# Kernel tuning notes

Measured on AMD Instinct MI355X. Metric: run time of the kernel, lower is better.

## Reference

```python
import math
import jax, jax.numpy as jnp
import numpy as np

ALPHA = 1000.0
N_LAMBDA = 1.0


def setup_inputs() -> dict:
    key = jax.random.key(0)
    k1, k2 = jax.random.split(key)
    xyz1 = jax.random.normal(k1, (4, 8192, 3), dtype=jnp.float32)  # prediction
    xyz2 = jax.random.normal(k2, (4, 8192, 3), dtype=jnp.float32)  # ground truth
    return {"xyz1": xyz1, "xyz2": xyz2}


def _nn(a, b):
    """For each point in a [B,Na,3], squared dist + index of nearest point in b [B,Nb,3]."""
    a2 = jnp.sum(a * a, axis=-1)[:, :, None]          # [B,Na,1]
    b2 = jnp.sum(b * b, axis=-1)[:, None, :]          # [B,1,Nb]
    d = a2 + b2 - 2.0 * jnp.einsum('bnd,bmd->bnm', a, b)  # [B,Na,Nb]
    return jnp.min(d, axis=-1), jnp.argmin(d, axis=-1)


def reference(xyz1, xyz2):
    B, n_x, _ = xyz1.shape
    n_gt = xyz2.shape[1]
    frac_21 = n_gt / n_x

    # torch code calls ChamferFunction.apply(xyz2, xyz1):
    # dist1/idx1 are for gt points (idx1 indexes into xyz1, range n_x),
    # dist2/idx2 are for pred points (idx2 indexes into xyz2, range n_gt).
    dist1, idx1 = _nn(xyz2, xyz1)   # [B, n_gt]
    dist2, idx2 = _nn(xyz1, xyz2)   # [B, n_x]

    exp_dist1 = jnp.exp(-dist1 * ALPHA)
    exp_dist2 = jnp.exp(-dist2 * ALPHA)

    batch = jnp.arange(B)[:, None]

    # how many gt points picked each pred point
    count1 = jnp.zeros((B, n_x), jnp.int32).at[batch, idx1].add(1)
    weight1 = jnp.take_along_axis(count1, idx1, axis=1).astype(jnp.float32) ** N_LAMBDA
    weight1 = 1.0 / jnp.maximum(frac_21 / weight1 + 1e-6, 1.0)
    loss1 = jnp.mean(1.0 - exp_dist1 * weight1, axis=1)

    # how many pred points picked each gt point
    count2 = jnp.zeros((B, n_gt), jnp.int32).at[batch, idx2].add(1)
    weight2 = jnp.take_along_axis(count2, idx2, axis=1).astype(jnp.float32) ** N_LAMBDA
    weight2 = 1.0 / (math.ceil(frac_21) * weight2 + 1e-6)
    loss2 = jnp.mean(1.0 - exp_dist2 * weight2, axis=1)

    return jnp.mean((loss1 + loss2) / 2.0)
```

## Files before the change

kernel.cpp:

```cpp
#include <hip/hip_runtime.h>
#include <cstdint>
#include <cstddef>

#define BATCH 4
#define NPTS 8192
#define CHUNK 128
#define BLOCK 256
#define QPT 8
#define QPB (BLOCK * QPT)
#define NKEYS (2 * BATCH * NPTS)

typedef float v2f __attribute__((ext_vector_type(2)));

__device__ __forceinline__ float halfnorm(float px, float py, float pz) {
    return 0.5f * fmaf(pz, pz, fmaf(py, py, px * px));
}
__device__ __forceinline__ float score(float qx, float qy, float qz,
                                       float px, float py, float pz, float ph) {
    float t = fmaf(-qx, px, ph);
    t = fmaf(-qy, py, t);
    return fmaf(-qz, pz, t);
}
__device__ __forceinline__ unsigned int mono_f32(float f) {
    unsigned int u = __float_as_uint(f);
    return u ^ (unsigned int)(((int)u >> 31) | 0x80000000);
}

__global__ void __launch_bounds__(BLOCK, 4) nn_kernel(
        const float* __restrict__ xyz1,
        const float* __restrict__ xyz2,
        unsigned long long* __restrict__ keys,
        unsigned int* __restrict__ counts,
        float* __restrict__ esum,
        float* __restrict__ out) {
    __shared__ float lx[CHUNK];
    __shared__ float ly[CHUNK];
    __shared__ float lz[CHUNK];
    __shared__ float lh[CHUNK];

    const int tid = threadIdx.x;
    const int qt  = blockIdx.x;
    const int ct  = blockIdx.y;
    const int zb  = blockIdx.z;
    const int b   = zb & 3;
    const int dir = zb >> 2;
    const float* q_ptr = (dir == 0) ? xyz2 : xyz1;
    const float* d_ptr = (dir == 0) ? xyz1 : xyz2;
    const int chunk0 = ct * CHUNK;

    {
        const int fid = (((zb * 64 + ct) * 4 + qt) * BLOCK) + tid;
        if (fid < NKEYS) {
            counts[fid] = 0u;
            esum[fid]   = 0.0f;
        }
        if (fid == 0) out[0] = 1.0f;
    }

    if (tid < 32) {
        const float4* g4 = (const float4*)(d_ptr + (size_t)(b * NPTS + chunk0) * 3);
        float4 t0 = g4[3 * tid + 0];
        float4 t1 = g4[3 * tid + 1];
        float4 t2 = g4[3 * tid + 2];
        float px[4] = {t0.x, t0.w, t1.z, t2.y};
        float py[4] = {t0.y, t1.x, t1.w, t2.z};
        float pz[4] = {t0.z, t1.y, t2.x, t2.w};
#pragma unroll
        for (int i = 0; i < 4; ++i) {
            lx[4 * tid + i] = px[i];
            ly[4 * tid + i] = py[i];
            lz[4 * tid + i] = pz[i];
            lh[4 * tid + i] = halfnorm(px[i], py[i], pz[i]);
        }
    }

    const int qbase = qt * QPB + tid;
    float qx[QPT], qy[QPT], qz[QPT];
#pragma unroll
    for (int u = 0; u < QPT; ++u) {
        const float* qp = q_ptr + (size_t)(b * NPTS + qbase + u * BLOCK) * 3;
        qx[u] = qp[0]; qy[u] = qp[1]; qz[u] = qp[2];
    }

    __syncthreads();

    float bd[QPT];
    int   bj[QPT];
#pragma unroll
    for (int u = 0; u < QPT; ++u) { bd[u] = 3.4e38f; bj[u] = 0; }

#pragma unroll 2
    for (int j = 0; j < CHUNK; j += 8) {
        float4 xa = *(const float4*)(lx + j);
        float4 xb = *(const float4*)(lx + j + 4);
        float4 ya = *(const float4*)(ly + j);
        float4 yb = *(const float4*)(ly + j + 4);
        float4 za = *(const float4*)(lz + j);
        float4 zb4 = *(const float4*)(lz + j + 4);
        float4 ha = *(const float4*)(lh + j);
        float4 hb = *(const float4*)(lh + j + 4);
        v2f x01 = {xa.x, xa.y}, x23 = {xa.z, xa.w}, x45 = {xb.x, xb.y}, x67 = {xb.z, xb.w};
        v2f y01 = {ya.x, ya.y}, y23 = {ya.z, ya.w}, y45 = {yb.x, yb.y}, y67 = {yb.z, yb.w};
        v2f z01 = {za.x, za.y}, z23 = {za.z, za.w}, z45 = {zb4.x, zb4.y}, z67 = {zb4.z, zb4.w};
        v2f h01 = {ha.x, ha.y}, h23 = {ha.z, ha.w}, h45 = {hb.x, hb.y}, h67 = {hb.z, hb.w};

#pragma unroll
        for (int u = 0; u < QPT; ++u) {
            const v2f nqx = {-qx[u], -qx[u]};
            const v2f nqy = {-qy[u], -qy[u]};
            const v2f nqz = {-qz[u], -qz[u]};
            v2f s01 = __builtin_elementwise_fma(nqx, x01, h01);
            v2f s23 = __builtin_elementwise_fma(nqx, x23, h23);
            v2f s45 = __builtin_elementwise_fma(nqx, x45, h45);
            v2f s67 = __builtin_elementwise_fma(nqx, x67, h67);
            s01 = __builtin_elementwise_fma(nqy, y01, s01);
            s23 = __builtin_elementwise_fma(nqy, y23, s23);
            s45 = __builtin_elementwise_fma(nqy, y45, s45);
            s67 = __builtin_elementwise_fma(nqy, y67, s67);
            s01 = __builtin_elementwise_fma(nqz, z01, s01);
            s23 = __builtin_elementwise_fma(nqz, z23, s23);
            s45 = __builtin_elementwise_fma(nqz, z45, s45);
            s67 = __builtin_elementwise_fma(nqz, z67, s67);

            float m0 = fminf(fminf(s01.x, s01.y), s23.x);
            float m1 = fminf(fminf(s23.y, s45.x), s45.y);
            float m2 = fminf(fminf(s67.x, s67.y), m0);
            float m  = fminf(m1, m2);
            if (m < bd[u]) { bd[u] = m; bj[u] = j; }
        }
    }

    const size_t base = ((size_t)zb) * NPTS;
#pragma unroll
    for (int u = 0; u < QPT; ++u) {
        unsigned long long key =
            ((unsigned long long)mono_f32(bd[u]) << 32) |
            (unsigned int)(chunk0 + bj[u]);
        atomicMin(&keys[base + qbase + u * BLOCK], key);
    }
}

__global__ void __launch_bounds__(BLOCK) mid_kernel(
        const float* __restrict__ xyz1,
        const float* __restrict__ xyz2,
        const unsigned long long* __restrict__ keys,
        unsigned int* __restrict__ counts,
        float* __restrict__ esum) {
    const int gtid = blockIdx.x * BLOCK + threadIdx.x;
    const int group = gtid >> 13;
    const int q   = gtid & (NPTS - 1);
    const int b   = group & 3;
    const int dir = group >> 2;
    const float* q_ptr = (dir == 0) ? xyz2 : xyz1;
    const float* d_ptr = (dir == 0) ? xyz1 : xyz2;

    const unsigned long long key = keys[gtid];
    const unsigned int smin_m = (unsigned int)(key >> 32);
    const int gbase = ((int)(unsigned int)key) & (NPTS - 8);

    const float* qp = q_ptr + (size_t)(b * NPTS + q) * 3;
    const float qx = qp[0], qy = qp[1], qz = qp[2];

    const float4* g4 = (const float4*)(d_ptr + (size_t)(b * NPTS + gbase) * 3);
    float4 t0 = g4[0], t1 = g4[1], t2 = g4[2], t3 = g4[3], t4 = g4[4], t5 = g4[5];
    float px[8] = {t0.x, t0.w, t1.z, t2.y, t3.x, t3.w, t4.z, t5.y};
    float py[8] = {t0.y, t1.x, t1.w, t2.z, t3.y, t4.x, t4.w, t5.z};
    float pz[8] = {t0.z, t1.y, t2.x, t2.w, t3.z, t4.y, t5.x, t5.w};

    int r = 0;
    float sx = px[0], sy = py[0], sz = pz[0];
#pragma unroll
    for (int k = 7; k >= 0; --k) {
        float ph = halfnorm(px[k], py[k], pz[k]);
        float s  = score(qx, qy, qz, px[k], py[k], pz[k], ph);
        if (mono_f32(s) == smin_m) { r = k; sx = px[k]; sy = py[k]; sz = pz[k]; }
    }
    const int idx = gbase + r;

    const float dx = qx - sx, dy = qy - sy, dz = qz - sz;
    const float d = dx * dx + dy * dy + dz * dz;
    const float e = expf(-1000.0f * d);

    atomicAdd(&counts[(size_t)group * NPTS + idx], 1u);
    atomicAdd(&esum[(size_t)group * NPTS + idx], e);
}

__global__ void __launch_bounds__(BLOCK) final_kernel(
        const unsigned int* __restrict__ counts,
        const float* __restrict__ esum,
        float* __restrict__ out) {
    __shared__ float red[4];
    const int gtid = blockIdx.x * BLOCK + threadIdx.x;
    const int dir = gtid >> 15;

    const float c = (float)counts[gtid];
    const float e = esum[gtid];
    float w;
    if (dir == 0) w = 1.0f / fmaxf(1.0f / c + 1e-6f, 1.0f);
    else          w = 1.0f / (c + 1e-6f);
    float term = -w * e;

#pragma unroll
    for (int off = 32; off > 0; off >>= 1)
        term += __shfl_down(term, off);
    const int lane = threadIdx.x & 63;
    const int wid  = threadIdx.x >> 6;
    if (lane == 0) red[wid] = term;
    __syncthreads();
    if (threadIdx.x == 0) {
        float t = red[0] + red[1] + red[2] + red[3];
        atomicAdd(out, t * (1.0f / 65536.0f));
    }
}

extern "C" void kernel_launch(void* const* d_in, const int* in_sizes, int n_in,
                              void* d_out, int out_size, void* d_ws, size_t ws_size,
                              hipStream_t stream) {
    const float* xyz1 = (const float*)d_in[0];
    const float* xyz2 = (const float*)d_in[1];
    float* out = (float*)d_out;

    unsigned long long* keys = (unsigned long long*)d_ws;
    unsigned int* counts = (unsigned int*)((char*)d_ws + (size_t)NKEYS * 8);
    float* esum = (float*)((char*)d_ws + (size_t)NKEYS * 12);

    nn_kernel<<<dim3(NPTS / QPB, NPTS / CHUNK, 2 * BATCH), BLOCK, 0, stream>>>(
        xyz1, xyz2, keys, counts, esum, out);
    mid_kernel<<<NKEYS / BLOCK, BLOCK, 0, stream>>>(xyz1, xyz2, keys, counts, esum);
    final_kernel<<<NKEYS / BLOCK, BLOCK, 0, stream>>>(counts, esum, out);
}
```

Measured before the change: 109.7 us.

## Precompute SoA coordinate planes and read candidates directly from global memory

Adds a prep kernel that converts both point clouds into structure-of-arrays planes with precomputed half-norms and also does the buffer zeroing. The NN kernel then reads candidate coordinates straight from these planes with block-uniform addresses instead of staging them through shared memory, which removes the LDS fill and the barrier. The cost is an extra kernel launch and extra global traffic for the planes.

```diff
diff --git a/kernel.cpp b/kernel.cpp
--- a/kernel.cpp
+++ b/kernel.cpp
@@ -26,18 +26,35 @@
     return u ^ (unsigned int)(((int)u >> 31) | 0x80000000);
 }
 
+__global__ void __launch_bounds__(BLOCK) prep_kernel(
+        const float* __restrict__ xyz1,
+        const float* __restrict__ xyz2,
+        float* __restrict__ planes,
+        unsigned int* __restrict__ counts,
+        float* __restrict__ esum,
+        float* __restrict__ out) {
+    const int gtid = blockIdx.x * BLOCK + threadIdx.x;
+    const int arr = gtid >> 15;
+    const int rem = gtid & 32767;
+    const int b = rem >> 13;
+    const int i = rem & (NPTS - 1);
+    const float* src = ((arr == 0) ? xyz1 : xyz2) + (size_t)(b * NPTS + i) * 3;
+    const float px = src[0], py = src[1], pz = src[2];
+    const size_t gb = ((size_t)(arr * 4 + b)) * 4 * NPTS;
+    planes[gb + 0 * NPTS + i] = px;
+    planes[gb + 1 * NPTS + i] = py;
+    planes[gb + 2 * NPTS + i] = pz;
+    planes[gb + 3 * NPTS + i] = halfnorm(px, py, pz);
+    counts[gtid] = 0u;
+    esum[gtid]   = 0.0f;
+    if (gtid == 0) out[0] = 1.0f;
+}
+
 __global__ void __launch_bounds__(BLOCK, 4) nn_kernel(
         const float* __restrict__ xyz1,
         const float* __restrict__ xyz2,
-        unsigned long long* __restrict__ keys,
-        unsigned int* __restrict__ counts,
-        float* __restrict__ esum,
-        float* __restrict__ out) {
-    __shared__ float lx[CHUNK];
-    __shared__ float ly[CHUNK];
-    __shared__ float lz[CHUNK];
-    __shared__ float lh[CHUNK];
-
+        const float* __restrict__ planes,
+        unsigned long long* __restrict__ keys) {
     const int tid = threadIdx.x;
     const int qt  = blockIdx.x;
     const int ct  = blockIdx.y;
@@ -45,34 +62,13 @@
     const int b   = zb & 3;
     const int dir = zb >> 2;
     const float* q_ptr = (dir == 0) ? xyz2 : xyz1;
-    const float* d_ptr = (dir == 0) ? xyz1 : xyz2;
+    const int g = (dir == 0) ? b : 4 + b;
     const int chunk0 = ct * CHUNK;
 
-    {
-        const int fid = (((zb * 64 + ct) * 4 + qt) * BLOCK) + tid;
-        if (fid < NKEYS) {
-            counts[fid] = 0u;
-            esum[fid]   = 0.0f;
-        }
-        if (fid == 0) out[0] = 1.0f;
-    }
-
-    if (tid < 32) {
-        const float4* g4 = (const float4*)(d_ptr + (size_t)(b * NPTS + chunk0) * 3);
-        float4 t0 = g4[3 * tid + 0];
-        float4 t1 = g4[3 * tid + 1];
-        float4 t2 = g4[3 * tid + 2];
-        float px[4] = {t0.x, t0.w, t1.z, t2.y};
-        float py[4] = {t0.y, t1.x, t1.w, t2.z};
-        float pz[4] = {t0.z, t1.y, t2.x, t2.w};
-#pragma unroll
-        for (int i = 0; i < 4; ++i) {
-            lx[4 * tid + i] = px[i];
-            ly[4 * tid + i] = py[i];
-            lz[4 * tid + i] = pz[i];
-            lh[4 * tid + i] = halfnorm(px[i], py[i], pz[i]);
-        }
-    }
+    const float* Xp = planes + ((size_t)g * 4 + 0) * NPTS + chunk0;
+    const float* Yp = planes + ((size_t)g * 4 + 1) * NPTS + chunk0;
+    const float* Zp = planes + ((size_t)g * 4 + 2) * NPTS + chunk0;
+    const float* Hp = planes + ((size_t)g * 4 + 3) * NPTS + chunk0;
 
     const int qbase = qt * QPB + tid;
     float qx[QPT], qy[QPT], qz[QPT];
@@ -82,8 +78,6 @@
         qx[u] = qp[0]; qy[u] = qp[1]; qz[u] = qp[2];
     }
 
-    __syncthreads();
-
     float bd[QPT];
     int   bj[QPT];
 #pragma unroll
@@ -91,18 +85,22 @@
 
 #pragma unroll 2
     for (int j = 0; j < CHUNK; j += 8) {
-        float4 xa = *(const float4*)(lx + j);
-        float4 xb = *(const float4*)(lx + j + 4);
-        float4 ya = *(const float4*)(ly + j);
-        float4 yb = *(const float4*)(ly + j + 4);
-        float4 za = *(const float4*)(lz + j);
-        float4 zb4 = *(const float4*)(lz + j + 4);
-        float4 ha = *(const float4*)(lh + j);
-        float4 hb = *(const float4*)(lh + j + 4);
-        v2f x01 = {xa.x, xa.y}, x23 = {xa.z, xa.w}, x45 = {xb.x, xb.y}, x67 = {xb.z, xb.w};
-        v2f y01 = {ya.x, ya.y}, y23 = {ya.z, ya.w}, y45 = {yb.x, yb.y}, y67 = {yb.z, yb.w};
-        v2f z01 = {za.x, za.y}, z23 = {za.z, za.w}, z45 = {zb4.x, zb4.y}, z67 = {zb4.z, zb4.w};
-        v2f h01 = {ha.x, ha.y}, h23 = {ha.z, ha.w}, h45 = {hb.x, hb.y}, h67 = {hb.z, hb.w};
+        const v2f x01 = *(const v2f*)(Xp + j);
+        const v2f x23 = *(const v2f*)(Xp + j + 2);
+        const v2f x45 = *(const v2f*)(Xp + j + 4);
+        const v2f x67 = *(const v2f*)(Xp + j + 6);
+        const v2f y01 = *(const v2f*)(Yp + j);
+        const v2f y23 = *(const v2f*)(Yp + j + 2);
+        const v2f y45 = *(const v2f*)(Yp + j + 4);
+        const v2f y67 = *(const v2f*)(Yp + j + 6);
+        const v2f z01 = *(const v2f*)(Zp + j);
+        const v2f z23 = *(const v2f*)(Zp + j + 2);
+        const v2f z45 = *(const v2f*)(Zp + j + 4);
+        const v2f z67 = *(const v2f*)(Zp + j + 6);
+        const v2f h01 = *(const v2f*)(Hp + j);
+        const v2f h23 = *(const v2f*)(Hp + j + 2);
+        const v2f h45 = *(const v2f*)(Hp + j + 4);
+        const v2f h67 = *(const v2f*)(Hp + j + 6);
 
 #pragma unroll
         for (int u = 0; u < QPT; ++u) {
@@ -223,9 +221,12 @@
     unsigned long long* keys = (unsigned long long*)d_ws;
     unsigned int* counts = (unsigned int*)((char*)d_ws + (size_t)NKEYS * 8);
     float* esum = (float*)((char*)d_ws + (size_t)NKEYS * 12);
-
+    float* planes = (float*)((char*)d_ws + (size_t)NKEYS * 16);
+
+    prep_kernel<<<NKEYS / BLOCK, BLOCK, 0, stream>>>(xyz1, xyz2, planes,
+                                                     counts, esum, out);
     nn_kernel<<<dim3(NPTS / QPB, NPTS / CHUNK, 2 * BATCH), BLOCK, 0, stream>>>(
-        xyz1, xyz2, keys, counts, esum, out);
+        xyz1, xyz2, planes, keys);
     mid_kernel<<<NKEYS / BLOCK, BLOCK, 0, stream>>>(xyz1, xyz2, keys, counts, esum);
     final_kernel<<<NKEYS / BLOCK, BLOCK, 0, stream>>>(counts, esum, out);
 }
```

After: 108.5 us. About the same (-1.1%).
